# Kernel tuning notes

Measured on AMD Instinct MI355X. Metric: run time of the kernel, lower is better.

## Reference

```python
import jax, jax.numpy as jnp
import numpy as np

N1D = 64   # 1D LUT knots per channel
M3D = 17   # 3D LUT grid size per axis
B, H, W = 4, 1024, 1024


def setup_inputs() -> dict:
    key = jax.random.key(0)
    kx, k1, k3 = jax.random.split(key, 3)
    x = jax.random.uniform(kx, (B, 3, H, W), dtype=jnp.float32)
    # learned LUTs: identity transform + small perturbation (realistic trained state)
    ramp = jnp.linspace(0.0, 1.0, N1D, dtype=jnp.float32)
    lut1d = jnp.tile(ramp[None, :], (3, 1)) + 0.02 * jax.random.normal(k1, (3, N1D), dtype=jnp.float32)
    g = jnp.linspace(0.0, 1.0, M3D, dtype=jnp.float32)
    rr, gg, bb = jnp.meshgrid(g, g, g, indexing='ij')
    lut3d = jnp.stack([rr, gg, bb], axis=-1) + 0.02 * jax.random.normal(k3, (M3D, M3D, M3D, 3), dtype=jnp.float32)
    return {"x": x, "lut1d": lut1d, "lut3d": lut3d}


def _apply_lut1d(x, lut1d):
    # x: [B,3,H,W] in [0,1]; lut1d: [3,N] per-channel curve, linear interp
    n = lut1d.shape[1]
    xs = x * (n - 1)
    i0 = jnp.clip(jnp.floor(xs).astype(jnp.int32), 0, n - 2)
    f = xs - i0.astype(x.dtype)
    v0 = jnp.stack([jnp.take(lut1d[c], i0[:, c]) for c in range(3)], axis=1)
    v1 = jnp.stack([jnp.take(lut1d[c], i0[:, c] + 1) for c in range(3)], axis=1)
    return v0 + f * (v1 - v0)


def _apply_lut3d(x, lut3d):
    # x: [B,3,H,W] in [0,1]; lut3d: [M,M,M,3] -> trilinear interpolation
    m = lut3d.shape[0]
    xs = x * (m - 1)
    i0 = jnp.clip(jnp.floor(xs).astype(jnp.int32), 0, m - 2)
    f = xs - i0.astype(x.dtype)
    ir, ig, ib = i0[:, 0], i0[:, 1], i0[:, 2]          # each [B,H,W]
    fr = f[:, 0, :, :, None]                            # [B,H,W,1]
    fg = f[:, 1, :, :, None]
    fb = f[:, 2, :, :, None]
    flat = lut3d.reshape(m * m * m, 3)

    def corner(dr, dg, db):
        lin = ((ir + dr) * m + (ig + dg)) * m + (ib + db)
        return flat[lin]                                # gather -> [B,H,W,3]

    out = (corner(0, 0, 0) * (1 - fr) * (1 - fg) * (1 - fb)
           + corner(1, 0, 0) * fr * (1 - fg) * (1 - fb)
           + corner(0, 1, 0) * (1 - fr) * fg * (1 - fb)
           + corner(0, 0, 1) * (1 - fr) * (1 - fg) * fb
           + corner(1, 1, 0) * fr * fg * (1 - fb)
           + corner(1, 0, 1) * fr * (1 - fg) * fb
           + corner(0, 1, 1) * (1 - fr) * fg * fb
           + corner(1, 1, 1) * fr * fg * fb)
    return jnp.moveaxis(out, -1, 1)                     # [B,3,H,W]


def reference(x, lut1d, lut3d):
    y = _apply_lut1d(x, lut1d)
    y = jnp.clip(y, 0.0, 1.0)
    return _apply_lut3d(y, lut3d)
```

## Files before the change

kernel.cpp:

```cpp
#include <hip/hip_runtime.h>
#include <hip/hip_fp16.h>

constexpr int kHW = 1024 * 1024;
constexpr int kB  = 4;
constexpr int kPairsPerImage = kHW / 2;
constexpr int kNPair = kB * kPairsPerImage;
constexpr int kM  = 17;
constexpr int kM3 = kM * kM * kM;

constexpr int kBlock = 512;
constexpr int kGrid  = 1024;

__device__ __forceinline__ float h2f_lo(unsigned int u) {
    __half2 h = *reinterpret_cast<__half2*>(&u);
    return __low2float(h);
}

__device__ __forceinline__ float apply1d(const float2* __restrict__ s1, int c, float v) {
    float xs = v * 63.0f;
    int i0 = (int)xs;
    i0 = min(max(i0, 0), 62);
    float f = xs - (float)i0;
    float2 p = s1[(c << 6) + i0];
    return fmaf(f, p.y - p.x, p.x);
}

struct F3 { float x, y, z; };

__device__ __forceinline__ F3 tri3d(const uint2* __restrict__ s3,
                                    float yr, float yg, float yb) {
    float xr = yr * 16.0f, xg = yg * 16.0f, xb = yb * 16.0f;
    int ir = min((int)xr, 15);
    int ig = min((int)xg, 15);
    int ib = min((int)xb, 15);
    float fr = xr - (float)ir;
    float fg = xg - (float)ig;
    float fb = xb - (float)ib;

    const int cell = (ir * 17 + ig) * 17 + ib;

    auto blerp = [&](const uint2* __restrict__ p) -> F3 {
        uint2 e0 = p[0];
        uint2 e1 = p[1];
        float2 a01 = __half22float2(*reinterpret_cast<__half2*>(&e0.x));
        float  a2  = h2f_lo(e0.y);
        float2 b01 = __half22float2(*reinterpret_cast<__half2*>(&e1.x));
        float  b2  = h2f_lo(e1.y);
        F3 r;
        r.x = fmaf(fb, b01.x - a01.x, a01.x);
        r.y = fmaf(fb, b01.y - a01.y, a01.y);
        r.z = fmaf(fb, b2 - a2, a2);
        return r;
    };

    F3 v00 = blerp(s3 + cell);
    F3 v01 = blerp(s3 + cell + 17);
    F3 v10 = blerp(s3 + cell + 289);
    F3 v11 = blerp(s3 + cell + 306);

    F3 v0, v1, vf;
    v0.x = fmaf(fg, v01.x - v00.x, v00.x);
    v0.y = fmaf(fg, v01.y - v00.y, v00.y);
    v0.z = fmaf(fg, v01.z - v00.z, v00.z);
    v1.x = fmaf(fg, v11.x - v10.x, v10.x);
    v1.y = fmaf(fg, v11.y - v10.y, v10.y);
    v1.z = fmaf(fg, v11.z - v10.z, v10.z);
    vf.x = fmaf(fr, v1.x - v0.x, v0.x);
    vf.y = fmaf(fr, v1.y - v0.y, v0.y);
    vf.z = fmaf(fr, v1.z - v0.z, v0.z);
    return vf;
}

__global__ __launch_bounds__(kBlock, 8) void lut_apply_kernel(
    const float* __restrict__ x,
    const float* __restrict__ lut1d,
    const float* __restrict__ lut3d,
    float* __restrict__ out)
{
    __shared__ uint2  s3[kM3];
    __shared__ float2 s1[3 * 64];

    for (int i = threadIdx.x; i < kM3; i += kBlock) {
        float c0 = lut3d[3 * i], c1 = lut3d[3 * i + 1], c2 = lut3d[3 * i + 2];
        __half2 h01 = __floats2half2_rn(c0, c1);
        __half2 h2p = __floats2half2_rn(c2, 0.0f);
        uint2 e;
        e.x = *reinterpret_cast<unsigned int*>(&h01);
        e.y = *reinterpret_cast<unsigned int*>(&h2p);
        s3[i] = e;
    }
    for (int i = threadIdx.x; i < 3 * 64; i += kBlock) {
        int c = i >> 6, j = i & 63;
        float a = lut1d[(c << 6) + j];
        float b = lut1d[(c << 6) + (j < 63 ? j + 1 : 63)];
        s1[i] = make_float2(a, b);
    }
    __syncthreads();

    const int tid = blockIdx.x * kBlock + threadIdx.x;
    const int nthreads = kGrid * kBlock;

    for (int q = tid; q < kNPair; q += nthreads) {
        const int b   = q >> 19;
        const int rem = q & (kPairsPerImage - 1);
        const size_t pR = (size_t)(b * 3 + 0) * kHW + 2 * (size_t)rem;
        const size_t pG = (size_t)(b * 3 + 1) * kHW + 2 * (size_t)rem;
        const size_t pB = (size_t)(b * 3 + 2) * kHW + 2 * (size_t)rem;

        const float2 r2 = *(const float2*)(x + pR);
        const float2 g2 = *(const float2*)(x + pG);
        const float2 b2 = *(const float2*)(x + pB);

        float ro[2], go[2], bo[2];
        const float rin[2] = {r2.x, r2.y};
        const float gin[2] = {g2.x, g2.y};
        const float bin[2] = {b2.x, b2.y};

        #pragma unroll
        for (int k = 0; k < 2; ++k) {
            float yr = apply1d(s1, 0, rin[k]);
            float yg = apply1d(s1, 1, gin[k]);
            float yb = apply1d(s1, 2, bin[k]);
            yr = fminf(fmaxf(yr, 0.0f), 1.0f);
            yg = fminf(fmaxf(yg, 0.0f), 1.0f);
            yb = fminf(fmaxf(yb, 0.0f), 1.0f);

            F3 v = tri3d(s3, yr, yg, yb);
            ro[k] = v.x; go[k] = v.y; bo[k] = v.z;
        }

        *(float2*)(out + pR) = make_float2(ro[0], ro[1]);
        *(float2*)(out + pG) = make_float2(go[0], go[1]);
        *(float2*)(out + pB) = make_float2(bo[0], bo[1]);
    }
}

extern "C" void kernel_launch(void* const* d_in, const int* in_sizes, int n_in,
                              void* d_out, int out_size, void* d_ws, size_t ws_size,
                              hipStream_t stream) {
    const float* x     = (const float*)d_in[0];
    const float* lut1d = (const float*)d_in[1];
    const float* lut3d = (const float*)d_in[2];
    float* out = (float*)d_out;

    hipLaunchKernelGGL(lut_apply_kernel, dim3(kGrid), dim3(kBlock), 0, stream,
                       x, lut1d, lut3d, out);
}
```

Measured before the change: 107.8 us.

## Use 128-bit nontemporal loads/stores and fully unroll two quads per thread

Replaces the grid-stride loop over pixel pairs with a fixed schedule in which each thread handles two quads of four pixels. Loads and stores become 128-bit nontemporal vector accesses, and all six loads are issued up front so more memory requests are in flight. The launch-bounds occupancy hint is dropped. In exchange the code now hard-codes the problem size to grid times block times eight pixels, and the higher register pressure may lower occupancy.

Measured after the change: 113.5 us. 1.05x slower.

```diff
diff --git a/kernel.cpp b/kernel.cpp
--- a/kernel.cpp
+++ b/kernel.cpp
@@ -3,13 +3,15 @@
 
 constexpr int kHW = 1024 * 1024;
 constexpr int kB  = 4;
-constexpr int kPairsPerImage = kHW / 2;
-constexpr int kNPair = kB * kPairsPerImage;
+constexpr int kQuadsPerImage = kHW / 4;
 constexpr int kM  = 17;
 constexpr int kM3 = kM * kM * kM;
 
-constexpr int kBlock = 512;
-constexpr int kGrid  = 1024;
+constexpr int kBlock   = 512;
+constexpr int kGrid    = 1024;
+constexpr int kThreads = kBlock * kGrid;
+
+typedef float f32x4 __attribute__((ext_vector_type(4)));
 
 __device__ __forceinline__ float h2f_lo(unsigned int u) {
     __half2 h = *reinterpret_cast<__half2*>(&u);
@@ -71,7 +73,26 @@
     return vf;
 }
 
-__global__ __launch_bounds__(kBlock, 8) void lut_apply_kernel(
+__device__ __forceinline__ void process_quad(const float2* __restrict__ s1,
+                                             const uint2*  __restrict__ s3,
+                                             f32x4 r4, f32x4 g4, f32x4 b4,
+                                             f32x4& ro, f32x4& go, f32x4& bo)
+{
+    #pragma unroll
+    for (int k = 0; k < 4; ++k) {
+        float yr = apply1d(s1, 0, r4[k]);
+        float yg = apply1d(s1, 1, g4[k]);
+        float yb = apply1d(s1, 2, b4[k]);
+        yr = fminf(fmaxf(yr, 0.0f), 1.0f);
+        yg = fminf(fmaxf(yg, 0.0f), 1.0f);
+        yb = fminf(fmaxf(yb, 0.0f), 1.0f);
+
+        F3 v = tri3d(s3, yr, yg, yb);
+        ro[k] = v.x; go[k] = v.y; bo[k] = v.z;
+    }
+}
+
+__global__ __launch_bounds__(kBlock) void lut_apply_kernel(
     const float* __restrict__ x,
     const float* __restrict__ lut1d,
     const float* __restrict__ lut3d,
@@ -97,42 +118,39 @@
     }
     __syncthreads();
 
-    const int tid = blockIdx.x * kBlock + threadIdx.x;
-    const int nthreads = kGrid * kBlock;
+    const int t = blockIdx.x * kBlock + threadIdx.x;
 
-    for (int q = tid; q < kNPair; q += nthreads) {
-        const int b   = q >> 19;
-        const int rem = q & (kPairsPerImage - 1);
-        const size_t pR = (size_t)(b * 3 + 0) * kHW + 2 * (size_t)rem;
-        const size_t pG = (size_t)(b * 3 + 1) * kHW + 2 * (size_t)rem;
-        const size_t pB = (size_t)(b * 3 + 2) * kHW + 2 * (size_t)rem;
+    const int q0 = t;
+    const int q1 = t + kThreads;
 
-        const float2 r2 = *(const float2*)(x + pR);
-        const float2 g2 = *(const float2*)(x + pG);
-        const float2 b2 = *(const float2*)(x + pB);
+    const int b0 = q0 >> 18, r0 = q0 & (kQuadsPerImage - 1);
+    const int b1 = q1 >> 18, r1 = q1 & (kQuadsPerImage - 1);
 
-        float ro[2], go[2], bo[2];
-        const float rin[2] = {r2.x, r2.y};
-        const float gin[2] = {g2.x, g2.y};
-        const float bin[2] = {b2.x, b2.y};
+    const size_t pR0 = (size_t)(b0 * 3 + 0) * kHW + 4 * (size_t)r0;
+    const size_t pG0 = (size_t)(b0 * 3 + 1) * kHW + 4 * (size_t)r0;
+    const size_t pB0 = (size_t)(b0 * 3 + 2) * kHW + 4 * (size_t)r0;
+    const size_t pR1 = (size_t)(b1 * 3 + 0) * kHW + 4 * (size_t)r1;
+    const size_t pG1 = (size_t)(b1 * 3 + 1) * kHW + 4 * (size_t)r1;
+    const size_t pB1 = (size_t)(b1 * 3 + 2) * kHW + 4 * (size_t)r1;
 
-        #pragma unroll
-        for (int k = 0; k < 2; ++k) {
-            float yr = apply1d(s1, 0, rin[k]);
-            float yg = apply1d(s1, 1, gin[k]);
-            float yb = apply1d(s1, 2, bin[k]);
-            yr = fminf(fmaxf(yr, 0.0f), 1.0f);
-            yg = fminf(fmaxf(yg, 0.0f), 1.0f);
-            yb = fminf(fmaxf(yb, 0.0f), 1.0f);
+    const f32x4 ar = __builtin_nontemporal_load((const f32x4*)(x + pR0));
+    const f32x4 ag = __builtin_nontemporal_load((const f32x4*)(x + pG0));
+    const f32x4 ab = __builtin_nontemporal_load((const f32x4*)(x + pB0));
+    const f32x4 cr = __builtin_nontemporal_load((const f32x4*)(x + pR1));
+    const f32x4 cg = __builtin_nontemporal_load((const f32x4*)(x + pG1));
+    const f32x4 cb = __builtin_nontemporal_load((const f32x4*)(x + pB1));
 
-            F3 v = tri3d(s3, yr, yg, yb);
-            ro[k] = v.x; go[k] = v.y; bo[k] = v.z;
-        }
+    f32x4 oR0, oG0, oB0;
+    process_quad(s1, s3, ar, ag, ab, oR0, oG0, oB0);
+    __builtin_nontemporal_store(oR0, (f32x4*)(out + pR0));
+    __builtin_nontemporal_store(oG0, (f32x4*)(out + pG0));
+    __builtin_nontemporal_store(oB0, (f32x4*)(out + pB0));
 
-        *(float2*)(out + pR) = make_float2(ro[0], ro[1]);
-        *(float2*)(out + pG) = make_float2(go[0], go[1]);
-        *(float2*)(out + pB) = make_float2(bo[0], bo[1]);
-    }
+    f32x4 oR1, oG1, oB1;
+    process_quad(s1, s3, cr, cg, cb, oR1, oG1, oB1);
+    __builtin_nontemporal_store(oR1, (f32x4*)(out + pR1));
+    __builtin_nontemporal_store(oG1, (f32x4*)(out + pG1));
+    __builtin_nontemporal_store(oB1, (f32x4*)(out + pB1));
 }
 
 extern "C" void kernel_launch(void* const* d_in, const int* in_sizes, int n_in,
```
